# Kernel optimization log

Measured on AMD Instinct MI355X. Metric: run time of the kernel, lower is better.

Reference implementation:

```python
import jax, jax.numpy as jnp
import numpy as np

B, S, D, H = 2, 2048, 1024, 16
DK = D // H
NEG = -1e9


def setup_inputs() -> dict:
    key = jax.random.key(0)
    ks = jax.random.split(key, 11)
    s = 1.0 / np.sqrt(D)
    inp = {
        "q": jax.random.normal(ks[0], (B, S, D), jnp.float32),
        "k": jax.random.normal(ks[1], (B, S, D), jnp.float32),
        "v": jax.random.normal(ks[2], (B, S, D), jnp.float32),
        "mask": jnp.tril(jnp.ones((S, S), jnp.int32))[None, None],  # [1,1,S,S] causal
        "Wq": jax.random.normal(ks[3], (D, D), jnp.float32) * s,
        "bq": jnp.zeros((D,), jnp.float32),
        "Wk": jax.random.normal(ks[4], (D, D), jnp.float32) * s,
        "bk": jnp.zeros((D,), jnp.float32),
        "Wv": jax.random.normal(ks[5], (D, D), jnp.float32) * s,
        "bv": jnp.zeros((D,), jnp.float32),
        "Wo": jax.random.normal(ks[6], (D, D), jnp.float32) * s,
        "bo": jnp.zeros((D,), jnp.float32),
    }
    return inp


def reference(q, k, v, mask, Wq, bq, Wk, bk, Wv, bv, Wo, bo):
    # projections (torch Linear: x @ W.T + b)
    Q = q @ Wq.T + bq
    K = k @ Wk.T + bk
    V = v @ Wv.T + bv
    # [B,S,D] -> [B,H,S,DK]
    Q = Q.reshape(B, S, H, DK).transpose(0, 2, 1, 3)
    K = K.reshape(B, S, H, DK).transpose(0, 2, 1, 3)
    V = V.reshape(B, S, H, DK).transpose(0, 2, 1, 3)
    scores = jnp.einsum("bhqd,bhkd->bhqk", Q, K) / jnp.sqrt(jnp.float32(DK))
    scores = jnp.where(mask == 0, jnp.float32(NEG), scores)
    attn = jax.nn.softmax(scores, axis=-1)  # dropout p=0.0 -> identity
    x = jnp.einsum("bhqk,bhkd->bhqd", attn, V)
    x = x.transpose(0, 2, 1, 3).reshape(B, S, D)
    return x @ Wo.T + bo
```

## Files before the change

### kernel.cpp

```cpp
#include <hip/hip_runtime.h>
#include <hip/hip_bf16.h>


typedef __bf16 bf16_t;
typedef __bf16 bf16x4 __attribute__((ext_vector_type(4)));
typedef __bf16 bf16x8 __attribute__((ext_vector_type(8)));
typedef float f32x4 __attribute__((ext_vector_type(4)));

#define BB 2
#define SS 2048
#define DD 1024
#define HH 16
#define DKK 64
#define MM 4096

#define NELT ((size_t)BB * SS * DD)
#define WELT ((size_t)DD * DD)

__device__ __align__(16) bf16_t g_ws[7 * NELT + 4 * WELT];

__device__ __forceinline__ void gld16(const bf16_t* g, bf16_t* l) {
    __builtin_amdgcn_global_load_lds(
        (const __attribute__((address_space(1))) void*)g,
        (__attribute__((address_space(3))) void*)l, 16, 0, 0);
}

__global__ __launch_bounds__(256) void cvt7(
    const float* __restrict__ q,  const float* __restrict__ k,  const float* __restrict__ v,
    const float* __restrict__ Wq, const float* __restrict__ Wk, const float* __restrict__ Wv,
    const float* __restrict__ Wo,
    bf16_t* __restrict__ qb, bf16_t* __restrict__ kb, bf16_t* __restrict__ vb,
    bf16_t* __restrict__ Wqb, bf16_t* __restrict__ Wkb, bf16_t* __restrict__ Wvb,
    bf16_t* __restrict__ Wob)
{
    const float* s; bf16_t* d; size_t n;
    switch (blockIdx.y) {
        case 0: s = q;  d = qb;  n = NELT; break;
        case 1: s = k;  d = kb;  n = NELT; break;
        case 2: s = v;  d = vb;  n = NELT; break;
        case 3: s = Wq; d = Wqb; n = WELT; break;
        case 4: s = Wk; d = Wkb; n = WELT; break;
        case 5: s = Wv; d = Wvb; n = WELT; break;
        default: s = Wo; d = Wob; n = WELT; break;
    }
    size_t e = ((size_t)blockIdx.x * 256 + threadIdx.x) * 8;
    if (e >= n) return;
    f32x4 a = *(const f32x4*)(s + e);
    f32x4 b = *(const f32x4*)(s + e + 4);
    bf16x8 o;
    #pragma unroll
    for (int i = 0; i < 4; ++i) { o[i] = (bf16_t)a[i]; o[4 + i] = (bf16_t)b[i]; }
    *(bf16x8*)(d + e) = o;
}

#define BM 128
#define BN 128
#define BK 32
#define LDC 136

__global__ __launch_bounds__(256) void gemm_qkv3(
    const bf16_t* __restrict__ qb, const bf16_t* __restrict__ kb, const bf16_t* __restrict__ vb,
    const bf16_t* __restrict__ Wqb, const bf16_t* __restrict__ Wkb, const bf16_t* __restrict__ Wvb,
    const float* __restrict__ bq, const float* __restrict__ bk, const float* __restrict__ bv,
    bf16_t* __restrict__ Qp, bf16_t* __restrict__ Kp, bf16_t* __restrict__ Vt)
{
    const int z = blockIdx.z;
    const bf16_t* A    = (z == 0) ? qb  : (z == 1) ? kb  : vb;
    const bf16_t* W    = (z == 0) ? Wqb : (z == 1) ? Wkb : Wvb;
    const float*  bias = (z == 0) ? bq  : (z == 1) ? bk  : bv;

    __shared__ __align__(16) bf16_t smem[128 * LDC];
    bf16_t (*As)[BK] = (bf16_t(*)[BK])smem;
    bf16_t (*Bs)[BK] = (bf16_t(*)[BK])(smem + 128 * BK);
    bf16_t (*Ct)[LDC] = (bf16_t(*)[LDC])smem;

    const int tid  = threadIdx.x;
    const int wave = tid >> 6;
    const int lane = tid & 63;
    const int quad = lane >> 4;
    const int c16  = lane & 15;
    const int bm = blockIdx.x * BM;
    const int bn = blockIdx.y * BN;
    const int wm = (wave >> 1) * 64;
    const int wn = (wave & 1) * 64;

    const int srow = wave * 16 + (lane >> 2);
    const int scol = (lane & 3) * 8;

    f32x4 acc[4][4] = {};

    for (int k0 = 0; k0 < DD; k0 += BK) {
        __syncthreads();
        #pragma unroll
        for (int rd = 0; rd < 2; ++rd) {
            gld16(A + (size_t)(bm + rd * 64 + srow) * DD + k0 + scol,
                  &As[rd * 64 + wave * 16][0]);
            gld16(W + (size_t)(bn + rd * 64 + srow) * DD + k0 + scol,
                  &Bs[rd * 64 + wave * 16][0]);
        }
        __syncthreads();

        bf16x8 af[4], bfr[4];
        #pragma unroll
        for (int tm = 0; tm < 4; ++tm)
            af[tm] = *(const bf16x8*)(&As[wm + tm * 16 + c16][quad * 8]);
        #pragma unroll
        for (int tn = 0; tn < 4; ++tn)
            bfr[tn] = *(const bf16x8*)(&Bs[wn + tn * 16 + c16][quad * 8]);

        #pragma unroll
        for (int tm = 0; tm < 4; ++tm)
            #pragma unroll
            for (int tn = 0; tn < 4; ++tn)
                acc[tm][tn] = __builtin_amdgcn_mfma_f32_16x16x32_bf16(
                    af[tm], bfr[tn], acc[tm][tn], 0, 0, 0);
    }

    float bia[4];
    #pragma unroll
    for (int tn = 0; tn < 4; ++tn)
        bia[tn] = bias[bn + wn + tn * 16 + c16];

    if (z < 2) {
        const float osc = (z == 0) ? 0.125f : 1.0f;
        bf16_t* C = (z == 0) ? Qp : Kp;
        #pragma unroll
        for (int tm = 0; tm < 4; ++tm)
            #pragma unroll
            for (int r = 0; r < 4; ++r) {
                size_t base = (size_t)(bm + wm + tm * 16 + quad * 4 + r) * DD;
                #pragma unroll
                for (int tn = 0; tn < 4; ++tn)
                    C[base + bn + wn + tn * 16 + c16] =
                        (bf16_t)((acc[tm][tn][r] + bia[tn]) * osc);
            }
    } else {
        __syncthreads();
        #pragma unroll
        for (int tm = 0; tm < 4; ++tm)
            #pragma unroll
            for (int tn = 0; tn < 4; ++tn) {
                bf16x4 pk;
                #pragma unroll
                for (int r = 0; r < 4; ++r)
                    pk[r] = (bf16_t)(acc[tm][tn][r] + bia[tn]);
                *(bf16x4*)(&Ct[wn + tn * 16 + c16][wm + tm * 16 + quad * 4]) = pk;
            }
        __syncthreads();
        const int b_    = bm >> 11;
        const int sbase = bm & (SS - 1);
        #pragma unroll
        for (int p = 0; p < 4; ++p) {
            int col = p * 32 + (tid >> 3);
            int si  = (tid & 7) * 8;
            size_t rowoff = (size_t)(b_ * 1024 + bn + col) * SS + sbase;
            #pragma unroll
            for (int half = 0; half < 2; ++half) {
                int s = si + half * 64;
                *(bf16x8*)(&Vt[rowoff + s]) = *(const bf16x8*)(&Ct[col][s]);
            }
        }
    }
}

__global__ __launch_bounds__(256) void gemm_out(
    const bf16_t* __restrict__ A,
    const bf16_t* __restrict__ W,
    const float* __restrict__ bias,
    float* __restrict__ C)
{
    __shared__ __align__(16) bf16_t As[BM][BK];
    __shared__ __align__(16) bf16_t Bs[BN][BK];

    const int tid  = threadIdx.x;
    const int wave = tid >> 6;
    const int lane = tid & 63;
    const int quad = lane >> 4;
    const int c16  = lane & 15;
    const int bm = blockIdx.x * BM;
    const int bn = blockIdx.y * BN;
    const int wm = (wave >> 1) * 64;
    const int wn = (wave & 1) * 64;

    const int srow = wave * 16 + (lane >> 2);
    const int scol = (lane & 3) * 8;

    f32x4 acc[4][4] = {};

    for (int k0 = 0; k0 < DD; k0 += BK) {
        __syncthreads();
        #pragma unroll
        for (int rd = 0; rd < 2; ++rd) {
            gld16(A + (size_t)(bm + rd * 64 + srow) * DD + k0 + scol,
                  &As[rd * 64 + wave * 16][0]);
            gld16(W + (size_t)(bn + rd * 64 + srow) * DD + k0 + scol,
                  &Bs[rd * 64 + wave * 16][0]);
        }
        __syncthreads();

        bf16x8 af[4], bfr[4];
        #pragma unroll
        for (int tm = 0; tm < 4; ++tm)
            af[tm] = *(const bf16x8*)(&As[wm + tm * 16 + c16][quad * 8]);
        #pragma unroll
        for (int tn = 0; tn < 4; ++tn)
            bfr[tn] = *(const bf16x8*)(&Bs[wn + tn * 16 + c16][quad * 8]);

        #pragma unroll
        for (int tm = 0; tm < 4; ++tm)
            #pragma unroll
            for (int tn = 0; tn < 4; ++tn)
                acc[tm][tn] = __builtin_amdgcn_mfma_f32_16x16x32_bf16(
                    af[tm], bfr[tn], acc[tm][tn], 0, 0, 0);
    }

    float bia[4];
    #pragma unroll
    for (int tn = 0; tn < 4; ++tn)
        bia[tn] = bias[bn + wn + tn * 16 + c16];

    #pragma unroll
    for (int tm = 0; tm < 4; ++tm)
        #pragma unroll
        for (int r = 0; r < 4; ++r) {
            size_t base = (size_t)(bm + wm + tm * 16 + quad * 4 + r) * DD;
            #pragma unroll
            for (int tn = 0; tn < 4; ++tn)
                C[base + bn + wn + tn * 16 + c16] = acc[tm][tn][r] + bia[tn];
        }
}

#define LDP 72

__global__ __launch_bounds__(256) void attn_fwd4(
    const bf16_t* __restrict__ Q,
    const bf16_t* __restrict__ K,
    const bf16_t* __restrict__ Vt,
    bf16_t* __restrict__ O)
{
    const int bh = blockIdx.y;
    const int b  = bh >> 4;
    const int h  = bh & 15;
    const int qbase = ((int)gridDim.x - 1 - (int)blockIdx.x) * 128;
    const int wave = threadIdx.x >> 6;
    const int lane = threadIdx.x & 63;
    const int quad = lane >> 4;
    const int c16  = lane & 15;

    __shared__ __align__(16) bf16_t Ps[4][32][LDP];

    const int qrow0w = qbase + wave * 32;
    const int kend   = qrow0w + 32;

    bf16x8 qf[2][2];
    #pragma unroll
    for (int tm = 0; tm < 2; ++tm) {
        const bf16_t* qp = Q + ((size_t)b * SS + qrow0w + tm * 16 + c16) * DD + h * DKK;
        qf[tm][0] = *(const bf16x8*)(qp + quad * 8);
        qf[tm][1] = *(const bf16x8*)(qp + 32 + quad * 8);
    }

    const bf16_t* Kb = K  + (size_t)b * SS * DD + h * DKK;
    const bf16_t* Vb = Vt + (size_t)(b * 1024 + h * DKK) * SS;

    f32x4 oacc[2][4] = {};
    float lsum[2][4] = {};

    bf16x8 kfA[4][2], kfB[4][2];
    #pragma unroll
    for (int ct = 0; ct < 4; ++ct) {
        const bf16_t* kp = Kb + (size_t)(ct * 16 + c16) * DD;
        kfA[ct][0] = *(const bf16x8*)(kp + quad * 8);
        kfA[ct][1] = *(const bf16x8*)(kp + 32 + quad * 8);
    }

    auto step = [&](int kb, bf16x8 (&kfc)[4][2], bf16x8 (&kfn)[4][2]) {
        f32x4 sc[2][4];
        #pragma unroll
        for (int tm = 0; tm < 2; ++tm)
            #pragma unroll
            for (int ct = 0; ct < 4; ++ct) {
                f32x4 s = {};
                s = __builtin_amdgcn_mfma_f32_16x16x32_bf16(qf[tm][0], kfc[ct][0], s, 0, 0, 0);
                s = __builtin_amdgcn_mfma_f32_16x16x32_bf16(qf[tm][1], kfc[ct][1], s, 0, 0, 0);
                sc[tm][ct] = s;
            }

        if (kb + 64 < kend) {
            #pragma unroll
            for (int ct = 0; ct < 4; ++ct) {
                const bf16_t* kp = Kb + (size_t)(kb + 64 + ct * 16 + c16) * DD;
                kfn[ct][0] = *(const bf16x8*)(kp + quad * 8);
                kfn[ct][1] = *(const bf16x8*)(kp + 32 + quad * 8);
            }
        }

        bf16x8 vf[4][2];
        #pragma unroll
        for (int tn = 0; tn < 4; ++tn) {
            const bf16_t* vp = Vb + (size_t)(tn * 16 + c16) * SS + kb;
            vf[tn][0] = *(const bf16x8*)(vp + quad * 8);
            vf[tn][1] = *(const bf16x8*)(vp + 32 + quad * 8);
        }

        #pragma unroll
        for (int tm = 0; tm < 2; ++tm) {
            int rbase = qrow0w + tm * 16 + quad * 4;
            #pragma unroll
            for (int ct = 0; ct < 4; ++ct) {
                int kidx = kb + ct * 16 + c16;
                #pragma unroll
                for (int r = 0; r < 4; ++r) {
                    float s = (kidx > rbase + r) ? -1e9f : sc[tm][ct][r];
                    float p = __expf(s);
                    Ps[wave][tm * 16 + quad * 4 + r][ct * 16 + c16] = (bf16_t)p;
                    lsum[tm][r] += p;
                }
            }
        }

        asm volatile("s_waitcnt lgkmcnt(0)" ::: "memory");

        #pragma unroll
        for (int tm = 0; tm < 2; ++tm) {
            bf16x8 pa0 = *(const bf16x8*)(&Ps[wave][tm * 16 + c16][quad * 8]);
            bf16x8 pa1 = *(const bf16x8*)(&Ps[wave][tm * 16 + c16][32 + quad * 8]);
            #pragma unroll
            for (int tn = 0; tn < 4; ++tn) {
                oacc[tm][tn] = __builtin_amdgcn_mfma_f32_16x16x32_bf16(pa0, vf[tn][0], oacc[tm][tn], 0, 0, 0);
                oacc[tm][tn] = __builtin_amdgcn_mfma_f32_16x16x32_bf16(pa1, vf[tn][1], oacc[tm][tn], 0, 0, 0);
            }
        }
    };

    for (int kb = 0; kb < kend; kb += 128) {
        step(kb, kfA, kfB);
        if (kb + 64 < kend) step(kb + 64, kfB, kfA);
    }

    #pragma unroll
    for (int tm = 0; tm < 2; ++tm)
        #pragma unroll
        for (int r = 0; r < 4; ++r) {
            float l = lsum[tm][r];
            #pragma unroll
            for (int off = 1; off < 16; off <<= 1)
                l += __shfl_xor(l, off, 64);
            float inv = 1.0f / l;
            int row = qrow0w + tm * 16 + quad * 4 + r;
            size_t base = ((size_t)b * SS + row) * DD + h * DKK;
            #pragma unroll
            for (int tn = 0; tn < 4; ++tn)
                O[base + tn * 16 + c16] = (bf16_t)(oacc[tm][tn][r] * inv);
        }
}

extern "C" void kernel_launch(void* const* d_in, const int* in_sizes, int n_in,
                              void* d_out, int out_size, void* d_ws, size_t ws_size,
                              hipStream_t stream) {
    (void)in_sizes; (void)n_in; (void)out_size; (void)d_ws; (void)ws_size;
    const float* q  = (const float*)d_in[0];
    const float* k  = (const float*)d_in[1];
    const float* v  = (const float*)d_in[2];
    const float* Wq = (const float*)d_in[4];
    const float* bq = (const float*)d_in[5];
    const float* Wk = (const float*)d_in[6];
    const float* bk = (const float*)d_in[7];
    const float* Wv = (const float*)d_in[8];
    const float* bv = (const float*)d_in[9];
    const float* Wo = (const float*)d_in[10];
    const float* bo = (const float*)d_in[11];

    bf16_t* ws;
    hipGetSymbolAddress((void**)&ws, HIP_SYMBOL(g_ws));
    bf16_t* Qp  = ws;
    bf16_t* Kp  = Qp + NELT;
    bf16_t* Vt  = Kp + NELT;
    bf16_t* Xa  = Vt + NELT;
    bf16_t* qb  = Xa + NELT;
    bf16_t* kb  = qb + NELT;
    bf16_t* vb  = kb + NELT;
    bf16_t* Wqb = vb + NELT;
    bf16_t* Wkb = Wqb + WELT;
    bf16_t* Wvb = Wkb + WELT;
    bf16_t* Wob = Wvb + WELT;

    cvt7<<<dim3(2048, 7), 256, 0, stream>>>(q, k, v, Wq, Wk, Wv, Wo,
                                            qb, kb, vb, Wqb, Wkb, Wvb, Wob);

    gemm_qkv3<<<dim3(MM / BM, DD / BN, 3), 256, 0, stream>>>(
        qb, kb, vb, Wqb, Wkb, Wvb, bq, bk, bv, Qp, Kp, Vt);

    attn_fwd4<<<dim3(SS / 128, BB * HH), 256, 0, stream>>>(Qp, Kp, Vt, Xa);

    gemm_out<<<dim3(MM / BM, DD / BN), 256, 0, stream>>>(Xa, Wob, bo, (float*)d_out);
}
```

Baseline: 326.4 us.

## Split attention keys across waves, widen GEMM K-tile, shrink output GEMM N-tile

Attention now gives each block 32 query rows, and its four waves take interleaved 32-key chunks. The per-wave partial outputs and row sums are then combined through shared memory. This launches four times as many blocks and balances the causal work across waves, which should raise occupancy and improve load balance. The cost is an extra shared-memory reduction and synchronisation, plus fewer MFMAs per key load. Separately, both GEMMs move to a 64-wide K tile to halve the barriers per K step, and the output GEMM uses 128x64 tiles to double its block count.

```diff
diff --git a/kernel.cpp b/kernel.cpp
--- a/kernel.cpp
+++ b/kernel.cpp
@@ -55,7 +55,7 @@
 
 #define BM 128
 #define BN 128
-#define BK 32
+#define BKG 64
 #define LDC 136
 
 __global__ __launch_bounds__(256) void gemm_qkv3(
@@ -70,8 +70,8 @@
     const float*  bias = (z == 0) ? bq  : (z == 1) ? bk  : bv;
 
     __shared__ __align__(16) bf16_t smem[128 * LDC];
-    bf16_t (*As)[BK] = (bf16_t(*)[BK])smem;
-    bf16_t (*Bs)[BK] = (bf16_t(*)[BK])(smem + 128 * BK);
+    bf16_t (*As)[BKG] = (bf16_t(*)[BKG])smem;
+    bf16_t (*Bs)[BKG] = (bf16_t(*)[BKG])(smem + 128 * BKG);
     bf16_t (*Ct)[LDC] = (bf16_t(*)[LDC])smem;
 
     const int tid  = threadIdx.x;
@@ -84,36 +84,37 @@
     const int wm = (wave >> 1) * 64;
     const int wn = (wave & 1) * 64;
 
-    const int srow = wave * 16 + (lane >> 2);
-    const int scol = (lane & 3) * 8;
+    const int srow = lane >> 3;
+    const int scol = (lane & 7) * 8;
 
     f32x4 acc[4][4] = {};
 
-    for (int k0 = 0; k0 < DD; k0 += BK) {
-        __syncthreads();
-        #pragma unroll
-        for (int rd = 0; rd < 2; ++rd) {
-            gld16(A + (size_t)(bm + rd * 64 + srow) * DD + k0 + scol,
-                  &As[rd * 64 + wave * 16][0]);
-            gld16(W + (size_t)(bn + rd * 64 + srow) * DD + k0 + scol,
-                  &Bs[rd * 64 + wave * 16][0]);
-        }
-        __syncthreads();
-
-        bf16x8 af[4], bfr[4];
-        #pragma unroll
-        for (int tm = 0; tm < 4; ++tm)
-            af[tm] = *(const bf16x8*)(&As[wm + tm * 16 + c16][quad * 8]);
-        #pragma unroll
-        for (int tn = 0; tn < 4; ++tn)
-            bfr[tn] = *(const bf16x8*)(&Bs[wn + tn * 16 + c16][quad * 8]);
-
-        #pragma unroll
-        for (int tm = 0; tm < 4; ++tm)
+    for (int k0 = 0; k0 < DD; k0 += BKG) {
+        __syncthreads();
+        #pragma unroll
+        for (int j = 0; j < 4; ++j) {
+            int r0 = wave * 32 + j * 8;
+            gld16(A + (size_t)(bm + r0 + srow) * DD + k0 + scol, &As[r0][0]);
+            gld16(W + (size_t)(bn + r0 + srow) * DD + k0 + scol, &Bs[r0][0]);
+        }
+        __syncthreads();
+
+        #pragma unroll
+        for (int ks = 0; ks < 2; ++ks) {
+            bf16x8 af[4], bfr[4];
+            #pragma unroll
+            for (int tm = 0; tm < 4; ++tm)
+                af[tm] = *(const bf16x8*)(&As[wm + tm * 16 + c16][ks * 32 + quad * 8]);
             #pragma unroll
             for (int tn = 0; tn < 4; ++tn)
-                acc[tm][tn] = __builtin_amdgcn_mfma_f32_16x16x32_bf16(
-                    af[tm], bfr[tn], acc[tm][tn], 0, 0, 0);
+                bfr[tn] = *(const bf16x8*)(&Bs[wn + tn * 16 + c16][ks * 32 + quad * 8]);
+            #pragma unroll
+            for (int tm = 0; tm < 4; ++tm)
+                #pragma unroll
+                for (int tn = 0; tn < 4; ++tn)
+                    acc[tm][tn] = __builtin_amdgcn_mfma_f32_16x16x32_bf16(
+                        af[tm], bfr[tn], acc[tm][tn], 0, 0, 0);
+        }
     }
 
     float bia[4];
@@ -169,54 +170,59 @@
     const float* __restrict__ bias,
     float* __restrict__ C)
 {
-    __shared__ __align__(16) bf16_t As[BM][BK];
-    __shared__ __align__(16) bf16_t Bs[BN][BK];
+    __shared__ __align__(16) bf16_t As[128][BKG];
+    __shared__ __align__(16) bf16_t Bs[64][BKG];
 
     const int tid  = threadIdx.x;
     const int wave = tid >> 6;
     const int lane = tid & 63;
     const int quad = lane >> 4;
     const int c16  = lane & 15;
-    const int bm = blockIdx.x * BM;
-    const int bn = blockIdx.y * BN;
+    const int bm = blockIdx.x * 128;
+    const int bn = blockIdx.y * 64;
     const int wm = (wave >> 1) * 64;
-    const int wn = (wave & 1) * 64;
-
-    const int srow = wave * 16 + (lane >> 2);
-    const int scol = (lane & 3) * 8;
-
-    f32x4 acc[4][4] = {};
-
-    for (int k0 = 0; k0 < DD; k0 += BK) {
-        __syncthreads();
-        #pragma unroll
-        for (int rd = 0; rd < 2; ++rd) {
-            gld16(A + (size_t)(bm + rd * 64 + srow) * DD + k0 + scol,
-                  &As[rd * 64 + wave * 16][0]);
-            gld16(W + (size_t)(bn + rd * 64 + srow) * DD + k0 + scol,
-                  &Bs[rd * 64 + wave * 16][0]);
-        }
-        __syncthreads();
-
-        bf16x8 af[4], bfr[4];
-        #pragma unroll
-        for (int tm = 0; tm < 4; ++tm)
-            af[tm] = *(const bf16x8*)(&As[wm + tm * 16 + c16][quad * 8]);
-        #pragma unroll
-        for (int tn = 0; tn < 4; ++tn)
-            bfr[tn] = *(const bf16x8*)(&Bs[wn + tn * 16 + c16][quad * 8]);
-
-        #pragma unroll
-        for (int tm = 0; tm < 4; ++tm)
-            #pragma unroll
-            for (int tn = 0; tn < 4; ++tn)
-                acc[tm][tn] = __builtin_amdgcn_mfma_f32_16x16x32_bf16(
-                    af[tm], bfr[tn], acc[tm][tn], 0, 0, 0);
-    }
-
-    float bia[4];
-    #pragma unroll
-    for (int tn = 0; tn < 4; ++tn)
+    const int wn = (wave & 1) * 32;
+
+    const int srow = lane >> 3;
+    const int scol = (lane & 7) * 8;
+
+    f32x4 acc[4][2] = {};
+
+    for (int k0 = 0; k0 < DD; k0 += BKG) {
+        __syncthreads();
+        #pragma unroll
+        for (int j = 0; j < 4; ++j) {
+            int r0 = wave * 32 + j * 8;
+            gld16(A + (size_t)(bm + r0 + srow) * DD + k0 + scol, &As[r0][0]);
+        }
+        #pragma unroll
+        for (int j = 0; j < 2; ++j) {
+            int r0 = wave * 16 + j * 8;
+            gld16(W + (size_t)(bn + r0 + srow) * DD + k0 + scol, &Bs[r0][0]);
+        }
+        __syncthreads();
+
+        #pragma unroll
+        for (int ks = 0; ks < 2; ++ks) {
+            bf16x8 af[4], bfr[2];
+            #pragma unroll
+            for (int tm = 0; tm < 4; ++tm)
+                af[tm] = *(const bf16x8*)(&As[wm + tm * 16 + c16][ks * 32 + quad * 8]);
+            #pragma unroll
+            for (int tn = 0; tn < 2; ++tn)
+                bfr[tn] = *(const bf16x8*)(&Bs[wn + tn * 16 + c16][ks * 32 + quad * 8]);
+            #pragma unroll
+            for (int tm = 0; tm < 4; ++tm)
+                #pragma unroll
+                for (int tn = 0; tn < 2; ++tn)
+                    acc[tm][tn] = __builtin_amdgcn_mfma_f32_16x16x32_bf16(
+                        af[tm], bfr[tn], acc[tm][tn], 0, 0, 0);
+        }
+    }
+
+    float bia[2];
+    #pragma unroll
+    for (int tn = 0; tn < 2; ++tn)
         bia[tn] = bias[bn + wn + tn * 16 + c16];
 
     #pragma unroll
@@ -225,14 +231,15 @@
         for (int r = 0; r < 4; ++r) {
             size_t base = (size_t)(bm + wm + tm * 16 + quad * 4 + r) * DD;
             #pragma unroll
-            for (int tn = 0; tn < 4; ++tn)
+            for (int tn = 0; tn < 2; ++tn)
                 C[base + bn + wn + tn * 16 + c16] = acc[tm][tn][r] + bia[tn];
         }
 }
 
-#define LDP 72
-
-__global__ __launch_bounds__(256) void attn_fwd4(
+#define LDPS 40
+#define LDOF 68
+
+__global__ __launch_bounds__(256) void attn_fwd5(
     const bf16_t* __restrict__ Q,
     const bf16_t* __restrict__ K,
     const bf16_t* __restrict__ Vt,
@@ -241,21 +248,23 @@
     const int bh = blockIdx.y;
     const int b  = bh >> 4;
     const int h  = bh & 15;
-    const int qbase = ((int)gridDim.x - 1 - (int)blockIdx.x) * 128;
+    const int qt = (int)gridDim.x - 1 - blockIdx.x;
+    const int qbase = qt * 32;
+    const int U = qt + 1;
     const int wave = threadIdx.x >> 6;
     const int lane = threadIdx.x & 63;
     const int quad = lane >> 4;
     const int c16  = lane & 15;
 
-    __shared__ __align__(16) bf16_t Ps[4][32][LDP];
-
-    const int qrow0w = qbase + wave * 32;
-    const int kend   = qrow0w + 32;
+    __shared__ __align__(16) unsigned char smraw[4 * 32 * LDOF * 4];
+    bf16_t (*Ps)[32][LDPS] = (bf16_t(*)[32][LDPS])smraw;
+    float  (*Of)[32][LDOF] = (float(*)[32][LDOF])smraw;
+    __shared__ float Ls[4][32];
 
     bf16x8 qf[2][2];
     #pragma unroll
     for (int tm = 0; tm < 2; ++tm) {
-        const bf16_t* qp = Q + ((size_t)b * SS + qrow0w + tm * 16 + c16) * DD + h * DKK;
+        const bf16_t* qp = Q + ((size_t)b * SS + qbase + tm * 16 + c16) * DD + h * DKK;
         qf[tm][0] = *(const bf16x8*)(qp + quad * 8);
         qf[tm][1] = *(const bf16x8*)(qp + 32 + quad * 8);
     }
@@ -266,52 +275,54 @@
     f32x4 oacc[2][4] = {};
     float lsum[2][4] = {};
 
-    bf16x8 kfA[4][2], kfB[4][2];
-    #pragma unroll
-    for (int ct = 0; ct < 4; ++ct) {
-        const bf16_t* kp = Kb + (size_t)(ct * 16 + c16) * DD;
-        kfA[ct][0] = *(const bf16x8*)(kp + quad * 8);
-        kfA[ct][1] = *(const bf16x8*)(kp + 32 + quad * 8);
-    }
-
-    auto step = [&](int kb, bf16x8 (&kfc)[4][2], bf16x8 (&kfn)[4][2]) {
-        f32x4 sc[2][4];
+    bf16x8 kfA[2][2], kfB[2][2];
+    {
+        int kb = wave * 32;
+        #pragma unroll
+        for (int ct = 0; ct < 2; ++ct) {
+            const bf16_t* kp = Kb + (size_t)(kb + ct * 16 + c16) * DD;
+            kfA[ct][0] = *(const bf16x8*)(kp + quad * 8);
+            kfA[ct][1] = *(const bf16x8*)(kp + 32 + quad * 8);
+        }
+    }
+
+    auto step = [&](int kb, bf16x8 (&kfc)[2][2], bf16x8 (&kfn)[2][2]) {
+        f32x4 sc[2][2];
         #pragma unroll
         for (int tm = 0; tm < 2; ++tm)
             #pragma unroll
-            for (int ct = 0; ct < 4; ++ct) {
+            for (int ct = 0; ct < 2; ++ct) {
                 f32x4 s = {};
                 s = __builtin_amdgcn_mfma_f32_16x16x32_bf16(qf[tm][0], kfc[ct][0], s, 0, 0, 0);
                 s = __builtin_amdgcn_mfma_f32_16x16x32_bf16(qf[tm][1], kfc[ct][1], s, 0, 0, 0);
                 sc[tm][ct] = s;
             }
 
-        if (kb + 64 < kend) {
-            #pragma unroll
-            for (int ct = 0; ct < 4; ++ct) {
-                const bf16_t* kp = Kb + (size_t)(kb + 64 + ct * 16 + c16) * DD;
+        if (kb + 128 < U * 32) {
+            #pragma unroll
+            for (int ct = 0; ct < 2; ++ct) {
+                const bf16_t* kp = Kb + (size_t)(kb + 128 + ct * 16 + c16) * DD;
                 kfn[ct][0] = *(const bf16x8*)(kp + quad * 8);
                 kfn[ct][1] = *(const bf16x8*)(kp + 32 + quad * 8);
             }
         }
 
-        bf16x8 vf[4][2];
-        #pragma unroll
-        for (int tn = 0; tn < 4; ++tn) {
-            const bf16_t* vp = Vb + (size_t)(tn * 16 + c16) * SS + kb;
-            vf[tn][0] = *(const bf16x8*)(vp + quad * 8);
-            vf[tn][1] = *(const bf16x8*)(vp + 32 + quad * 8);
-        }
-
+        bf16x8 vf[4];
+        #pragma unroll
+        for (int tn = 0; tn < 4; ++tn)
+            vf[tn] = *(const bf16x8*)(Vb + (size_t)(tn * 16 + c16) * SS + kb + quad * 8);
+
+        const bool needmask = (kb >= qbase);
         #pragma unroll
         for (int tm = 0; tm < 2; ++tm) {
-            int rbase = qrow0w + tm * 16 + quad * 4;
-            #pragma unroll
-            for (int ct = 0; ct < 4; ++ct) {
+            int rbase = qbase + tm * 16 + quad * 4;
+            #pragma unroll
+            for (int ct = 0; ct < 2; ++ct) {
                 int kidx = kb + ct * 16 + c16;
                 #pragma unroll
                 for (int r = 0; r < 4; ++r) {
-                    float s = (kidx > rbase + r) ? -1e9f : sc[tm][ct][r];
+                    float s = sc[tm][ct][r];
+                    if (needmask && kidx > rbase + r) s = -1e9f;
                     float p = __expf(s);
                     Ps[wave][tm * 16 + quad * 4 + r][ct * 16 + c16] = (bf16_t)p;
                     lsum[tm][r] += p;
@@ -323,20 +334,32 @@
 
         #pragma unroll
         for (int tm = 0; tm < 2; ++tm) {
-            bf16x8 pa0 = *(const bf16x8*)(&Ps[wave][tm * 16 + c16][quad * 8]);
-            bf16x8 pa1 = *(const bf16x8*)(&Ps[wave][tm * 16 + c16][32 + quad * 8]);
-            #pragma unroll
-            for (int tn = 0; tn < 4; ++tn) {
-                oacc[tm][tn] = __builtin_amdgcn_mfma_f32_16x16x32_bf16(pa0, vf[tn][0], oacc[tm][tn], 0, 0, 0);
-                oacc[tm][tn] = __builtin_amdgcn_mfma_f32_16x16x32_bf16(pa1, vf[tn][1], oacc[tm][tn], 0, 0, 0);
-            }
+            bf16x8 pa = *(const bf16x8*)(&Ps[wave][tm * 16 + c16][quad * 8]);
+            #pragma unroll
+            for (int tn = 0; tn < 4; ++tn)
+                oacc[tm][tn] = __builtin_amdgcn_mfma_f32_16x16x32_bf16(
+                    pa, vf[tn], oacc[tm][tn], 0, 0, 0);
         }
     };
 
-    for (int kb = 0; kb < kend; kb += 128) {
-        step(kb, kfA, kfB);
-        if (kb + 64 < kend) step(kb + 64, kfB, kfA);
-    }
+    {
+        int u = wave; bool cur = false;
+        while (u < U) {
+            if (!cur) step(u * 32, kfA, kfB);
+            else      step(u * 32, kfB, kfA);
+            u += 4; cur = !cur;
+        }
+    }
+
+    __syncthreads();
+
+    #pragma unroll
+    for (int tm = 0; tm < 2; ++tm)
+        #pragma unroll
+        for (int tn = 0; tn < 4; ++tn)
+            #pragma unroll
+            for (int r = 0; r < 4; ++r)
+                Of[wave][tm * 16 + quad * 4 + r][tn * 16 + c16] = oacc[tm][tn][r];
 
     #pragma unroll
     for (int tm = 0; tm < 2; ++tm)
@@ -346,13 +369,29 @@
             #pragma unroll
             for (int off = 1; off < 16; off <<= 1)
                 l += __shfl_xor(l, off, 64);
-            float inv = 1.0f / l;
-            int row = qrow0w + tm * 16 + quad * 4 + r;
-            size_t base = ((size_t)b * SS + row) * DD + h * DKK;
-            #pragma unroll
-            for (int tn = 0; tn < 4; ++tn)
-                O[base + tn * 16 + c16] = (bf16_t)(oacc[tm][tn][r] * inv);
-        }
+            if (c16 == 0) Ls[wave][tm * 16 + quad * 4 + r] = l;
+        }
+    __syncthreads();
+
+    {
+        int row = wave * 8 + (lane >> 3);
+        int col = (lane & 7) * 8;
+        float l = Ls[0][row] + Ls[1][row] + Ls[2][row] + Ls[3][row];
+        f32x4 s0 = {}, s1 = {};
+        #pragma unroll
+        for (int p = 0; p < 4; ++p) {
+            s0 += *(const f32x4*)(&Of[p][row][col]);
+            s1 += *(const f32x4*)(&Of[p][row][col + 4]);
+        }
+        float inv = 1.0f / l;
+        bf16x8 o;
+        #pragma unroll
+        for (int i = 0; i < 4; ++i) {
+            o[i]     = (bf16_t)(s0[i] * inv);
+            o[4 + i] = (bf16_t)(s1[i] * inv);
+        }
+        *(bf16x8*)(&O[((size_t)b * SS + qbase + row) * DD + h * DKK + col]) = o;
+    }
 }
 
 extern "C" void kernel_launch(void* const* d_in, const int* in_sizes, int n_in,
@@ -391,7 +430,7 @@
     gemm_qkv3<<<dim3(MM / BM, DD / BN, 3), 256, 0, stream>>>(
         qb, kb, vb, Wqb, Wkb, Wvb, bq, bk, bv, Qp, Kp, Vt);
 
-    attn_fwd4<<<dim3(SS / 128, BB * HH), 256, 0, stream>>>(Qp, Kp, Vt, Xa);
-
-    gemm_out<<<dim3(MM / BM, DD / BN), 256, 0, stream>>>(Xa, Wob, bo, (float*)d_out);
-}
+    attn_fwd5<<<dim3(SS / 32, BB * HH), 256, 0, stream>>>(Qp, Kp, Vt, Xa);
+
+    gemm_out<<<dim3(MM / 128, DD / 64), 256, 0, stream>>>(Xa, Wob, bo, (float*)d_out);
+}
```

Result: faster. 312.2 us (-4.3%).
